# Optimization experiments

Measured on AMD Instinct MI355X. Metric: run time of the kernel, lower is better.

The kernel has to match this reference:

```python
import jax, jax.numpy as jnp
import numpy as np

K = 512       # embedding dim (also per-head dim in this quirky impl)
H = 8         # heads
NB = 4        # transformer blocks
VOCAB = 32000
BATCH = 4
T = 512
EPS = 1e-5


def setup_inputs() -> dict:
    key = jax.random.key(0)
    ks = jax.random.split(key, 16)
    s = 0.02
    f = jnp.float32
    return {
        "x": jax.random.randint(ks[0], (BATCH, T), 0, VOCAB, dtype=jnp.int64) if jax.config.jax_enable_x64 else jax.random.randint(ks[0], (BATCH, T), 0, VOCAB, dtype=jnp.int32),
        "embed_W": (jax.random.normal(ks[1], (VOCAB, K)) * s).astype(f),
        "Wq": (jax.random.normal(ks[2], (NB, K, K * H)) * s).astype(f),
        "Wk": (jax.random.normal(ks[3], (NB, K, K * H)) * s).astype(f),
        "Wv": (jax.random.normal(ks[4], (NB, K, K * H)) * s).astype(f),
        "Wu": (jax.random.normal(ks[5], (NB, K * H, K)) * s).astype(f),
        "bu": jnp.zeros((NB, K), f),
        "W1": (jax.random.normal(ks[6], (NB, K, 4 * K)) * s).astype(f),
        "b1": jnp.zeros((NB, 4 * K), f),
        "W2": (jax.random.normal(ks[7], (NB, 4 * K, K)) * s).astype(f),
        "b2": jnp.zeros((NB, K), f),
        "ln1_w": jnp.ones((NB, K), f), "ln1_b": jnp.zeros((NB, K), f),
        "ln2_w": jnp.ones((NB, K), f), "ln2_b": jnp.zeros((NB, K), f),
        "lnf_w": jnp.ones((K,), f),    "lnf_b": jnp.zeros((K,), f),
        "unembed_W": (jax.random.normal(ks[8], (K, VOCAB)) * s).astype(f),
        "unembed_b": jnp.zeros((VOCAB,), f),
    }


def _layernorm(x, w, b):
    m = jnp.mean(x, axis=-1, keepdims=True)
    v = jnp.mean((x - m) ** 2, axis=-1, keepdims=True)
    return (x - m) / jnp.sqrt(v + EPS) * w + b


def _pos_encoding(t, k):
    pos = jnp.arange(t, dtype=jnp.float32)[:, None]
    # faithful to source: div = 10000 ** (2 * arange(0,k,2) / k)
    div = 10000.0 ** (2.0 * jnp.arange(0, k, 2, dtype=jnp.float32) / k)
    ang = pos / div  # [t, k//2]
    y = jnp.zeros((t, k), jnp.float32)
    y = y.at[:, 0::2].set(jnp.sin(ang)).at[:, 1::2].set(jnp.cos(ang))
    return y


def _block(h, Wq, Wk, Wv, Wu, bu, W1, b1, W2, b2, ln1_w, ln1_b, ln2_w, ln2_b):
    b, t, k = h.shape
    q = (h @ Wq).reshape(b, t, H, k)
    kk = (h @ Wk).reshape(b, t, H, k)
    v = (h @ Wv).reshape(b, t, H, k)
    scores = jnp.einsum('bqhd,bshd->bhqs', q, kk) / (k ** 0.5)
    causal = jnp.tril(jnp.ones((t, t), bool))  # keep lower triangle
    scores = jnp.where(causal[None, None], scores, -jnp.inf)
    att = jax.nn.softmax(scores, axis=-1)
    y = jnp.einsum('bhqs,bshd->bqhd', att, v).reshape(b, t, H * k)
    y = y @ Wu + bu
    h = _layernorm(y + h, ln1_w, ln1_b)          # residual + norm1 (dropout off)
    ff = jax.nn.gelu(h @ W1 + b1, approximate=False) @ W2 + b2
    return _layernorm(ff + h, ln2_w, ln2_b)       # residual + norm2


def reference(x, embed_W, Wq, Wk, Wv, Wu, bu, W1, b1, W2, b2,
              ln1_w, ln1_b, ln2_w, ln2_b, lnf_w, lnf_b, unembed_W, unembed_b):
    b, t = x.shape
    h = embed_W[x] + _pos_encoding(t, K)
    for i in range(NB):
        h = _block(h, Wq[i], Wk[i], Wv[i], Wu[i], bu[i], W1[i], b1[i], W2[i], b2[i],
                   ln1_w[i], ln1_b[i], ln2_w[i], ln2_b[i])
    h = _layernorm(h, lnf_w, lnf_b)
    # torch does .squeeze(0): no-op for b>1, so output is [b, t, vocab]
    return h @ unembed_W + unembed_b
```

## Files before the change

kernel.cpp:

```cpp
#include <hip/hip_runtime.h>
#include <math.h>
#include <stdint.h>

#define KDIM 512
#define HEADS 8
#define NBLK 4
#define TSEQ 512
#define BATCH_ 4
#define ROWS 2048
#define DMODEL 4096
#define VOCAB_ 32000
#define FFDIM 2048

typedef __attribute__((ext_vector_type(4))) float f32x4;
typedef __attribute__((ext_vector_type(8))) short s16x8;
typedef unsigned short u16t;

__device__ __forceinline__ u16t f2bf(float f) {
    union { float f; unsigned u; } cv; cv.f = f;
    return (u16t)((cv.u + 0x7FFFu + ((cv.u >> 16) & 1u)) >> 16);
}

__device__ __forceinline__ void gload_lds16(const void* g, void* lds) {
    __builtin_amdgcn_global_load_lds(
        (const __attribute__((address_space(1))) unsigned int*)(uintptr_t)g,
        (__attribute__((address_space(3))) unsigned int*)(unsigned int)(uintptr_t)lds,
        16, 0, 0);
}

template<int BM, int BN, bool OUTBF, bool BIAS, bool GELU, bool MASK, bool KTRI>
__global__ __launch_bounds__(256, 2) void gemm_bf16(
    const u16t* __restrict__ A, const u16t* __restrict__ Bt,
    const float* __restrict__ bias, void* __restrict__ Cv,
    int Kd, int lda, int ldb, int ldc,
    long long aSB, long long aSH, long long bSB, long long bSH,
    long long cSB, long long cSH, int Hn, float scale)
{
    const int m0 = blockIdx.y * BM, n0 = blockIdx.x * BN;
    if (MASK && n0 > m0) return;

    const int zb = blockIdx.z / Hn, zh = blockIdx.z % Hn;
    A  += zb * aSB + zh * aSH;
    Bt += zb * bSB + zh * bSH;
    const int tid = threadIdx.x;
    const int wave = tid >> 6, lane = tid & 63;
    const int quad = lane >> 4, l15 = lane & 15;
    const int wm = (wave >> 1) * (BM / 2), wn = (wave & 1) * (BN / 2);
    constexpr int MT = BM / 32, NT = BN / 32;

    __shared__ __align__(16) u16t As[BM * 64];
    __shared__ __align__(16) u16t Bs[BN * 64];

    f32x4 acc[MT][NT];
    #pragma unroll
    for (int i = 0; i < MT; i++)
        #pragma unroll
        for (int j = 0; j < NT; j++)
            acc[i][j] = (f32x4){0.f, 0.f, 0.f, 0.f};

    const int kend = KTRI ? (Kd < m0 + BM ? Kd : m0 + BM) : Kd;

    for (int k0 = 0; k0 < kend; k0 += 64) {
        #pragma unroll
        for (int r = 0; r < BM / 32; ++r) {
            int cc = r * 256 + tid;
            int row = cc >> 3, pc = cc & 7;
            int kc = pc ^ (row & 7);
            gload_lds16(A + (long long)(m0 + row) * lda + k0 + kc * 8, &As[cc * 8]);
        }
        #pragma unroll
        for (int r = 0; r < BN / 32; ++r) {
            int cc = r * 256 + tid;
            int row = cc >> 3, pc = cc & 7;
            int kc = pc ^ (row & 7);
            gload_lds16(Bt + (long long)(n0 + row) * ldb + k0 + kc * 8, &Bs[cc * 8]);
        }
        __syncthreads();

        #pragma unroll
        for (int g = 0; g < 2; ++g) {
            s16x8 af[MT], bfr[NT];
            #pragma unroll
            for (int i = 0; i < MT; i++) {
                int row = wm + i * 16 + l15;
                int pc = (g * 4 + quad) ^ (row & 7);
                af[i] = *(const s16x8*)&As[row * 64 + pc * 8];
            }
            #pragma unroll
            for (int j = 0; j < NT; j++) {
                int row = wn + j * 16 + l15;
                int pc = (g * 4 + quad) ^ (row & 7);
                bfr[j] = *(const s16x8*)&Bs[row * 64 + pc * 8];
            }
            #pragma unroll
            for (int i = 0; i < MT; i++)
                #pragma unroll
                for (int j = 0; j < NT; j++)
                    acc[i][j] = __builtin_amdgcn_mfma_f32_16x16x32_bf16(
                        af[i], bfr[j], acc[i][j], 0, 0, 0);
        }
        __syncthreads();
    }

    const long long cb = zb * cSB + zh * cSH;
    #pragma unroll
    for (int i = 0; i < MT; i++) {
        #pragma unroll
        for (int j = 0; j < NT; j++) {
            const int col = n0 + wn + j * 16 + l15;
            #pragma unroll
            for (int r = 0; r < 4; r++) {
                const int row = m0 + wm + i * 16 + quad * 4 + r;
                float v = acc[i][j][r] * scale;
                if (BIAS) v += bias[col];
                if (GELU) v = 0.5f * v * (1.0f + erff(v * 0.70710678118654752f));
                if (OUTBF) ((u16t*)Cv)[cb + (long long)row * ldc + col] = f2bf(v);
                else       ((float*)Cv)[cb + (long long)row * ldc + col] = v;
            }
        }
    }
}

__global__ __launch_bounds__(256) void wconvT(
    const float* __restrict__ W, int ldw, int n_off, long long srcZ,
    u16t* __restrict__ WT, int ldt, long long dstZ)
{
    W  += (long long)blockIdx.z * srcZ;
    WT += (long long)blockIdx.z * dstZ;
    __shared__ float t[32][33];
    const int n0 = blockIdx.x * 32, k0 = blockIdx.y * 32;
    const int c = threadIdx.x & 31, r = threadIdx.x >> 5;
    #pragma unroll
    for (int i = 0; i < 4; i++)
        t[r + i * 8][c] = W[(long long)(k0 + r + i * 8) * ldw + n_off + n0 + c];
    __syncthreads();
    #pragma unroll
    for (int i = 0; i < 4; i++)
        WT[(long long)(n0 + r + i * 8) * ldt + k0 + c] = f2bf(t[c][r + i * 8]);
}

__global__ __launch_bounds__(256) void embed_pos(
    const int* __restrict__ x, const float* __restrict__ W,
    float* __restrict__ h, u16t* __restrict__ hb)
{
    int idx = blockIdx.x * 256 + threadIdx.x;
    int row = idx >> 9, c = idx & 511;
    int tpos = row & (TSEQ - 1);
    int tok = x[row];
    int i = c >> 1;
    float inv = expf(-9.210340371976184f * ((float)i * (1.0f / 128.0f)));
    float ang = (float)tpos * inv;
    float pe = (c & 1) ? cosf(ang) : sinf(ang);
    float v = W[(long long)tok * KDIM + c] + pe;
    h[idx] = v;
    hb[idx] = f2bf(v);
}

template<int NP, bool GB, bool RES>
__global__ __launch_bounds__(64) void ln512(
    const float* __restrict__ A, const float* __restrict__ R,
    const float* __restrict__ gb,
    const float* __restrict__ w, const float* __restrict__ bias,
    float* __restrict__ out, u16t* __restrict__ outb)
{
    long long row = blockIdx.x;
    int t = threadIdx.x;
    const float* a = A + row * KDIM;
    float4 u0 = *(const float4*)&a[t * 4];
    float4 u1 = *(const float4*)&a[256 + t * 4];
    if (NP == 2) {
        const float* a2 = A + (long long)ROWS * KDIM + row * KDIM;
        float4 p0 = *(const float4*)&a2[t * 4];
        float4 p1 = *(const float4*)&a2[256 + t * 4];
        u0.x += p0.x; u0.y += p0.y; u0.z += p0.z; u0.w += p0.w;
        u1.x += p1.x; u1.y += p1.y; u1.z += p1.z; u1.w += p1.w;
    }
    if (GB) {
        float4 g0 = *(const float4*)&gb[t * 4];
        float4 g1 = *(const float4*)&gb[256 + t * 4];
        u0.x += g0.x; u0.y += g0.y; u0.z += g0.z; u0.w += g0.w;
        u1.x += g1.x; u1.y += g1.y; u1.z += g1.z; u1.w += g1.w;
    }
    if (RES) {
        const float* rr = R + row * KDIM;
        float4 r0 = *(const float4*)&rr[t * 4];
        float4 r1 = *(const float4*)&rr[256 + t * 4];
        u0.x += r0.x; u0.y += r0.y; u0.z += r0.z; u0.w += r0.w;
        u1.x += r1.x; u1.y += r1.y; u1.z += r1.z; u1.w += r1.w;
    }
    float xv[8] = {u0.x, u0.y, u0.z, u0.w, u1.x, u1.y, u1.z, u1.w};
    float s = 0.f;
    #pragma unroll
    for (int e = 0; e < 8; e++) s += xv[e];
    #pragma unroll
    for (int off = 32; off; off >>= 1) s += __shfl_xor(s, off);
    float mean = s * (1.0f / 512.0f);
    float vs = 0.f;
    #pragma unroll
    for (int e = 0; e < 8; e++) { float d = xv[e] - mean; vs += d * d; }
    #pragma unroll
    for (int off = 32; off; off >>= 1) vs += __shfl_xor(vs, off);
    float rstd = rsqrtf(vs * (1.0f / 512.0f) + 1e-5f);

    int c0 = t * 4, c1 = 256 + t * 4;
    #pragma unroll
    for (int e = 0; e < 8; e++) {
        int c = (e < 4) ? (c0 + e) : (c1 + e - 4);
        float o = (xv[e] - mean) * rstd * w[c] + bias[c];
        out[row * KDIM + c] = o;
        outb[row * KDIM + c] = f2bf(o);
    }
}

__global__ __launch_bounds__(64) void softmax512b(
    const float* __restrict__ S, u16t* __restrict__ P)
{
    long long base = (long long)blockIdx.x * 512;
    const int r = blockIdx.x & (TSEQ - 1);
    int t = threadIdx.x;
    float4 u0 = *(const float4*)&S[base + t * 4];
    float4 u1 = *(const float4*)&S[base + 256 + t * 4];
    float xv[8] = {u0.x, u0.y, u0.z, u0.w, u1.x, u1.y, u1.z, u1.w};
    #pragma unroll
    for (int e = 0; e < 8; e++) {
        int c = (e < 4) ? (t * 4 + e) : (256 + t * 4 + e - 4);
        if (c > r) xv[e] = -1e30f;
    }
    float m = xv[0];
    #pragma unroll
    for (int e = 1; e < 8; e++) m = fmaxf(m, xv[e]);
    #pragma unroll
    for (int off = 32; off; off >>= 1) m = fmaxf(m, __shfl_xor(m, off));
    float s = 0.f;
    #pragma unroll
    for (int e = 0; e < 8; e++) { xv[e] = expf(xv[e] - m); s += xv[e]; }
    #pragma unroll
    for (int off = 32; off; off >>= 1) s += __shfl_xor(s, off);
    float inv = 1.0f / s;
    #pragma unroll
    for (int e = 0; e < 8; e++) {
        int c = (e < 4) ? (t * 4 + e) : (256 + t * 4 + e - 4);
        P[base + c] = f2bf(xv[e] * inv);
    }
}

extern "C" void kernel_launch(void* const* d_in, const int* in_sizes, int n_in,
                              void* d_out, int out_size, void* d_ws, size_t ws_size,
                              hipStream_t stream)
{
    const int*   x      = (const int*)  d_in[0];
    const float* embedW = (const float*)d_in[1];
    const float* Wq     = (const float*)d_in[2];
    const float* Wk     = (const float*)d_in[3];
    const float* Wv     = (const float*)d_in[4];
    const float* Wu     = (const float*)d_in[5];
    const float* bu     = (const float*)d_in[6];
    const float* W1     = (const float*)d_in[7];
    const float* b1     = (const float*)d_in[8];
    const float* W2     = (const float*)d_in[9];
    const float* b2     = (const float*)d_in[10];
    const float* ln1w   = (const float*)d_in[11];
    const float* ln1b   = (const float*)d_in[12];
    const float* ln2w   = (const float*)d_in[13];
    const float* ln2b   = (const float*)d_in[14];
    const float* lnfw   = (const float*)d_in[15];
    const float* lnfb   = (const float*)d_in[16];
    const float* unembW = (const float*)d_in[17];
    const float* unembB = (const float*)d_in[18];

    char* ob = (char*)d_out;
    float* outF = (float*)d_out;

    u16t*  wb  = (u16t*)(ob);
    u16t*  qk  = (u16t*)(ob + 83886080);
    u16t*  vt  = (u16t*)(ob + 117440512);
    float* sc  = (float*)(ob + 134217728);
    u16t*  Pb  = (u16t*) (ob + 167772160);
    u16t*  y   = (u16t*) (ob + 184549376);
    u16t*  f1  = (u16t*) (ob + 201326592);
    float* tmp = (float*)(ob + 209715200);
    float* ff2 = (float*)(ob + 218103808);
    float* h   = (float*)(ob + 226492416);
    float* h2  = (float*)(ob + 230686720);
    u16t*  hb  = (u16t*) (ob + 234881024);
    u16t*  h2b = (u16t*) (ob + 236978176);

    char* wsb = (char*)d_ws;
    u16t* hf  = (u16t*)(wsb);
    u16t* wun = (u16t*)(wsb + 2097152);

    const long long WBLK = 10485760;
    const long long OQ = 0, OK_ = 2097152, OV = 4194304, OU = 6291456,
                    O1 = 8388608, O2 = 9437184;

    const float inv_sqrt_k = 0.04419417382415922f;
    const long long z0 = 0;

    wconvT<<<dim3(DMODEL/32, KDIM/32, NBLK), 256, 0, stream>>>(
        Wq, DMODEL, 0, (long long)KDIM*DMODEL, wb + OQ, KDIM, WBLK);
    wconvT<<<dim3(DMODEL/32, KDIM/32, NBLK), 256, 0, stream>>>(
        Wk, DMODEL, 0, (long long)KDIM*DMODEL, wb + OK_, KDIM, WBLK);
    wconvT<<<dim3(DMODEL/32, KDIM/32, NBLK), 256, 0, stream>>>(
        Wv, DMODEL, 0, (long long)KDIM*DMODEL, wb + OV, KDIM, WBLK);
    wconvT<<<dim3(KDIM/32, DMODEL/32, NBLK), 256, 0, stream>>>(
        Wu, KDIM, 0, (long long)DMODEL*KDIM, wb + OU, DMODEL, WBLK);
    wconvT<<<dim3(FFDIM/32, KDIM/32, NBLK), 256, 0, stream>>>(
        W1, FFDIM, 0, (long long)KDIM*FFDIM, wb + O1, KDIM, WBLK);
    wconvT<<<dim3(KDIM/32, FFDIM/32, NBLK), 256, 0, stream>>>(
        W2, KDIM, 0, (long long)FFDIM*KDIM, wb + O2, FFDIM, WBLK);

    embed_pos<<<ROWS * KDIM / 256, 256, 0, stream>>>(x, embedW, h, hb);

    for (int i = 0; i < NBLK; i++) {
        u16t* wbi = wb + (long long)i * WBLK;

        gemm_bf16<128,128,true,false,false,false,false>
            <<<dim3(64, 16, 1), 256, 0, stream>>>(
            hb, wbi + OQ, nullptr, qk, KDIM, KDIM, KDIM, 2*DMODEL,
            z0,z0,z0,z0,z0,z0, 1, 1.0f);

        gemm_bf16<128,128,true,false,false,false,false>
            <<<dim3(16, 32, 1), 256, 0, stream>>>(
            wbi + OV, hb, nullptr, vt, KDIM, KDIM, KDIM, ROWS,
            z0,z0,z0,z0,z0,z0, 1, 1.0f);

        gemm_bf16<128,128,false,false,false,true,false>
            <<<dim3(4, 4, BATCH_*HEADS), 256, 0, stream>>>(
            qk, qk + DMODEL, nullptr, sc, KDIM, 2*DMODEL, 2*DMODEL, TSEQ,
            (long long)TSEQ*2*DMODEL, (long long)KDIM,
            (long long)TSEQ*2*DMODEL, (long long)KDIM,
            (long long)HEADS*TSEQ*TSEQ, (long long)TSEQ*TSEQ, HEADS, inv_sqrt_k);

        softmax512b<<<BATCH_*HEADS*TSEQ, 64, 0, stream>>>(sc, Pb);

        gemm_bf16<128,128,true,false,false,false,true>
            <<<dim3(4, 4, BATCH_*HEADS), 256, 0, stream>>>(
            Pb, vt, nullptr, y, TSEQ, TSEQ, ROWS, DMODEL,
            (long long)HEADS*TSEQ*TSEQ, (long long)TSEQ*TSEQ,
            (long long)TSEQ, (long long)TSEQ*ROWS,
            (long long)TSEQ*DMODEL, (long long)KDIM, HEADS, 1.0f);

        gemm_bf16<64,64,false,false,false,false,false>
            <<<dim3(8, 32, 2), 256, 0, stream>>>(
            y, wbi + OU, nullptr, tmp, DMODEL/2, DMODEL, DMODEL, KDIM,
            (long long)(DMODEL/2), z0, (long long)(DMODEL/2), z0,
            (long long)ROWS*KDIM, z0, 1, 1.0f);

        ln512<2,true,true><<<ROWS, 64, 0, stream>>>(
            tmp, h, bu + i*KDIM, ln1w + i*KDIM, ln1b + i*KDIM, h2, h2b);

        gemm_bf16<64,128,true,true,true,false,false>
            <<<dim3(16, 32, 1), 256, 0, stream>>>(
            h2b, wbi + O1, b1 + i*FFDIM, f1, KDIM, KDIM, KDIM, FFDIM,
            z0,z0,z0,z0,z0,z0, 1, 1.0f);

        gemm_bf16<64,64,false,false,false,false,false>
            <<<dim3(8, 32, 2), 256, 0, stream>>>(
            f1, wbi + O2, nullptr, ff2, FFDIM/2, FFDIM, FFDIM, KDIM,
            (long long)(FFDIM/2), z0, (long long)(FFDIM/2), z0,
            (long long)ROWS*KDIM, z0, 1, 1.0f);

        ln512<2,true,true><<<ROWS, 64, 0, stream>>>(
            ff2, h2, b2 + i*KDIM, ln2w + i*KDIM, ln2b + i*KDIM, h, hb);
    }

    ln512<1,false,false><<<ROWS, 64, 0, stream>>>(
        h, nullptr, nullptr, lnfw, lnfb, tmp, hf);

    const int CH = 6400;
    for (int c = 0; c < 5; c++) {
        wconvT<<<dim3(CH/32, KDIM/32, 1), 256, 0, stream>>>(
            unembW, VOCAB_, c*CH, z0, wun, KDIM, z0);
        gemm_bf16<128,128,false,true,false,false,false>
            <<<dim3(CH/128, 16, 1), 256, 0, stream>>>(
            hf, wun, unembB + c*CH, outF + c*CH, KDIM, KDIM, KDIM, VOCAB_,
            z0,z0,z0,z0,z0,z0, 1, 1.0f);
    }
}
```

Before: 1.182 ms.

## Fuse QKV projection and weight conversions, widen split-K, batch row kernels

Merges the Q/K and V-transpose projection GEMMs into one launch and the three Wq/Wk/Wv conversion kernels into one. The Wu projection moves to 128x128 tiles with split-K of 8 into the scores buffer, and LN1 sums the eight partials. LayerNorm and softmax now process four rows per 256-thread block. The diagonal-heavy P·V tiles are launched first (reversed row order). When workspace allows, unembedding runs as a single conversion and GEMM instead of five chunks. Together these cut launch count and tail effects, at the cost of more partial-sum traffic.

```diff
diff --git a/kernel.cpp b/kernel.cpp
--- a/kernel.cpp
+++ b/kernel.cpp
@@ -28,20 +28,13 @@
         16, 0, 0);
 }
 
-template<int BM, int BN, bool OUTBF, bool BIAS, bool GELU, bool MASK, bool KTRI>
-__global__ __launch_bounds__(256, 2) void gemm_bf16(
+template<int BM, int BN, bool OUTBF, bool BIAS, bool GELU, bool KTRI>
+__device__ __forceinline__ void gemm_body(
     const u16t* __restrict__ A, const u16t* __restrict__ Bt,
     const float* __restrict__ bias, void* __restrict__ Cv,
-    int Kd, int lda, int ldb, int ldc,
-    long long aSB, long long aSH, long long bSB, long long bSH,
-    long long cSB, long long cSH, int Hn, float scale)
-{
-    const int m0 = blockIdx.y * BM, n0 = blockIdx.x * BN;
-    if (MASK && n0 > m0) return;
-
-    const int zb = blockIdx.z / Hn, zh = blockIdx.z % Hn;
-    A  += zb * aSB + zh * aSH;
-    Bt += zb * bSB + zh * bSH;
+    int Kd, int lda, int ldb, int ldc, long long cb,
+    int m0, int n0, float scale)
+{
     const int tid = threadIdx.x;
     const int wave = tid >> 6, lane = tid & 63;
     const int quad = lane >> 4, l15 = lane & 15;
@@ -102,7 +95,6 @@
         __syncthreads();
     }
 
-    const long long cb = zb * cSB + zh * cSH;
     #pragma unroll
     for (int i = 0; i < MT; i++) {
         #pragma unroll
@@ -121,6 +113,42 @@
     }
 }
 
+template<int BM, int BN, bool OUTBF, bool BIAS, bool GELU, bool MASK, bool KTRI>
+__global__ __launch_bounds__(256, 2) void gemm_bf16(
+    const u16t* __restrict__ A, const u16t* __restrict__ Bt,
+    const float* __restrict__ bias, void* __restrict__ Cv,
+    int Kd, int lda, int ldb, int ldc,
+    long long aSB, long long aSH, long long bSB, long long bSH,
+    long long cSB, long long cSH, int Hn, float scale)
+{
+    const int by = KTRI ? (gridDim.y - 1 - blockIdx.y) : blockIdx.y;
+    const int m0 = by * BM, n0 = blockIdx.x * BN;
+    if (MASK && n0 > m0) return;
+    const int zb = blockIdx.z / Hn, zh = blockIdx.z % Hn;
+    gemm_body<BM, BN, OUTBF, BIAS, GELU, KTRI>(
+        A + zb * aSB + zh * aSH, Bt + zb * bSB + zh * bSH, bias, Cv,
+        Kd, lda, ldb, ldc, zb * cSB + zh * cSH, m0, n0, scale);
+}
+
+__global__ __launch_bounds__(256, 2) void gemm_qkvt(
+    const u16t* __restrict__ hb, const u16t* __restrict__ wq,
+    u16t* __restrict__ qk, const u16t* __restrict__ wv,
+    u16t* __restrict__ vt)
+{
+    const int bx = blockIdx.x;
+    const u16t* A; const u16t* Bt; u16t* C; int ldc, m0, n0;
+    if (bx < 1024) {
+        A = hb; Bt = wq; C = qk; ldc = 2 * DMODEL;
+        n0 = (bx & 63) * 128; m0 = (bx >> 6) * 128;
+    } else {
+        int i = bx - 1024;
+        A = wv; Bt = hb; C = vt; ldc = ROWS;
+        n0 = (i & 15) * 128; m0 = (i >> 4) * 128;
+    }
+    gemm_body<128, 128, true, false, false, false>(
+        A, Bt, nullptr, C, KDIM, KDIM, KDIM, ldc, 0, m0, n0, 1.0f);
+}
+
 __global__ __launch_bounds__(256) void wconvT(
     const float* __restrict__ W, int ldw, int n_off, long long srcZ,
     u16t* __restrict__ WT, int ldt, long long dstZ)
@@ -132,11 +160,31 @@
     const int c = threadIdx.x & 31, r = threadIdx.x >> 5;
     #pragma unroll
     for (int i = 0; i < 4; i++)
-        t[r + i * 8][c] = W[(long long)(k0 + r + i * 8) * ldw + n_off + n0 + c];
+        t[r + i * 8][c] = W[(long long)(k0 + r + i * 8) * ldw + n0 + c + n_off];
     __syncthreads();
     #pragma unroll
     for (int i = 0; i < 4; i++)
         WT[(long long)(n0 + r + i * 8) * ldt + k0 + c] = f2bf(t[c][r + i * 8]);
+}
+
+__global__ __launch_bounds__(256) void wconvT3(
+    const float* __restrict__ W0, const float* __restrict__ W1,
+    const float* __restrict__ W2, long long srcZ,
+    u16t* __restrict__ WT, long long dstZ, long long dstG)
+{
+    const int zi = blockIdx.z >> 2, zb = blockIdx.z & 3;
+    const float* W = (zi == 0 ? W0 : zi == 1 ? W1 : W2) + zb * srcZ;
+    u16t* D = WT + zi * dstG + zb * dstZ;
+    __shared__ float t[32][33];
+    const int n0 = blockIdx.x * 32, k0 = blockIdx.y * 32;
+    const int c = threadIdx.x & 31, r = threadIdx.x >> 5;
+    #pragma unroll
+    for (int i = 0; i < 4; i++)
+        t[r + i * 8][c] = W[(long long)(k0 + r + i * 8) * DMODEL + n0 + c];
+    __syncthreads();
+    #pragma unroll
+    for (int i = 0; i < 4; i++)
+        D[(long long)(n0 + r + i * 8) * KDIM + k0 + c] = f2bf(t[c][r + i * 8]);
 }
 
 __global__ __launch_bounds__(256) void embed_pos(
@@ -157,21 +205,22 @@
 }
 
 template<int NP, bool GB, bool RES>
-__global__ __launch_bounds__(64) void ln512(
+__global__ __launch_bounds__(256) void ln512(
     const float* __restrict__ A, const float* __restrict__ R,
     const float* __restrict__ gb,
     const float* __restrict__ w, const float* __restrict__ bias,
     float* __restrict__ out, u16t* __restrict__ outb)
 {
-    long long row = blockIdx.x;
-    int t = threadIdx.x;
+    const int wv = threadIdx.x >> 6, t = threadIdx.x & 63;
+    long long row = (long long)blockIdx.x * 4 + wv;
     const float* a = A + row * KDIM;
     float4 u0 = *(const float4*)&a[t * 4];
     float4 u1 = *(const float4*)&a[256 + t * 4];
-    if (NP == 2) {
-        const float* a2 = A + (long long)ROWS * KDIM + row * KDIM;
-        float4 p0 = *(const float4*)&a2[t * 4];
-        float4 p1 = *(const float4*)&a2[256 + t * 4];
+    #pragma unroll
+    for (int p = 1; p < NP; ++p) {
+        const float* ap = a + (long long)p * ROWS * KDIM;
+        float4 p0 = *(const float4*)&ap[t * 4];
+        float4 p1 = *(const float4*)&ap[256 + t * 4];
         u0.x += p0.x; u0.y += p0.y; u0.z += p0.z; u0.w += p0.w;
         u1.x += p1.x; u1.y += p1.y; u1.z += p1.z; u1.w += p1.w;
     }
@@ -212,12 +261,13 @@
     }
 }
 
-__global__ __launch_bounds__(64) void softmax512b(
+__global__ __launch_bounds__(256) void softmax512b(
     const float* __restrict__ S, u16t* __restrict__ P)
 {
-    long long base = (long long)blockIdx.x * 512;
-    const int r = blockIdx.x & (TSEQ - 1);
-    int t = threadIdx.x;
+    const int wv = threadIdx.x >> 6, t = threadIdx.x & 63;
+    long long row = (long long)blockIdx.x * 4 + wv;
+    long long base = row * 512;
+    const int r = (int)(row & (TSEQ - 1));
     float4 u0 = *(const float4*)&S[base + t * 4];
     float4 u1 = *(const float4*)&S[base + 256 + t * 4];
     float xv[8] = {u0.x, u0.y, u0.z, u0.w, u1.x, u1.y, u1.z, u1.w};
@@ -278,30 +328,26 @@
     u16t*  Pb  = (u16t*) (ob + 167772160);
     u16t*  y   = (u16t*) (ob + 184549376);
     u16t*  f1  = (u16t*) (ob + 201326592);
-    float* tmp = (float*)(ob + 209715200);
     float* ff2 = (float*)(ob + 218103808);
     float* h   = (float*)(ob + 226492416);
     float* h2  = (float*)(ob + 230686720);
     u16t*  hb  = (u16t*) (ob + 234881024);
     u16t*  h2b = (u16t*) (ob + 236978176);
+    float* tmp = sc;
 
     char* wsb = (char*)d_ws;
     u16t* hf  = (u16t*)(wsb);
     u16t* wun = (u16t*)(wsb + 2097152);
 
     const long long WBLK = 10485760;
-    const long long OQ = 0, OK_ = 2097152, OV = 4194304, OU = 6291456,
+    const long long OQ = 0, OV = 4194304, OU = 6291456,
                     O1 = 8388608, O2 = 9437184;
 
     const float inv_sqrt_k = 0.04419417382415922f;
     const long long z0 = 0;
 
-    wconvT<<<dim3(DMODEL/32, KDIM/32, NBLK), 256, 0, stream>>>(
-        Wq, DMODEL, 0, (long long)KDIM*DMODEL, wb + OQ, KDIM, WBLK);
-    wconvT<<<dim3(DMODEL/32, KDIM/32, NBLK), 256, 0, stream>>>(
-        Wk, DMODEL, 0, (long long)KDIM*DMODEL, wb + OK_, KDIM, WBLK);
-    wconvT<<<dim3(DMODEL/32, KDIM/32, NBLK), 256, 0, stream>>>(
-        Wv, DMODEL, 0, (long long)KDIM*DMODEL, wb + OV, KDIM, WBLK);
+    wconvT3<<<dim3(DMODEL/32, KDIM/32, 3*NBLK), 256, 0, stream>>>(
+        Wq, Wk, Wv, (long long)KDIM*DMODEL, wb, WBLK, 2097152);
     wconvT<<<dim3(KDIM/32, DMODEL/32, NBLK), 256, 0, stream>>>(
         Wu, KDIM, 0, (long long)DMODEL*KDIM, wb + OU, DMODEL, WBLK);
     wconvT<<<dim3(FFDIM/32, KDIM/32, NBLK), 256, 0, stream>>>(
@@ -314,15 +360,8 @@
     for (int i = 0; i < NBLK; i++) {
         u16t* wbi = wb + (long long)i * WBLK;
 
-        gemm_bf16<128,128,true,false,false,false,false>
-            <<<dim3(64, 16, 1), 256, 0, stream>>>(
-            hb, wbi + OQ, nullptr, qk, KDIM, KDIM, KDIM, 2*DMODEL,
-            z0,z0,z0,z0,z0,z0, 1, 1.0f);
-
-        gemm_bf16<128,128,true,false,false,false,false>
-            <<<dim3(16, 32, 1), 256, 0, stream>>>(
-            wbi + OV, hb, nullptr, vt, KDIM, KDIM, KDIM, ROWS,
-            z0,z0,z0,z0,z0,z0, 1, 1.0f);
+        gemm_qkvt<<<dim3(1536, 1, 1), 256, 0, stream>>>(
+            hb, wbi + OQ, qk, wbi + OV, vt);
 
         gemm_bf16<128,128,false,false,false,true,false>
             <<<dim3(4, 4, BATCH_*HEADS), 256, 0, stream>>>(
@@ -331,7 +370,7 @@
             (long long)TSEQ*2*DMODEL, (long long)KDIM,
             (long long)HEADS*TSEQ*TSEQ, (long long)TSEQ*TSEQ, HEADS, inv_sqrt_k);
 
-        softmax512b<<<BATCH_*HEADS*TSEQ, 64, 0, stream>>>(sc, Pb);
+        softmax512b<<<BATCH_*HEADS*TSEQ/4, 256, 0, stream>>>(sc, Pb);
 
         gemm_bf16<128,128,true,false,false,false,true>
             <<<dim3(4, 4, BATCH_*HEADS), 256, 0, stream>>>(
@@ -340,13 +379,13 @@
             (long long)TSEQ, (long long)TSEQ*ROWS,
             (long long)TSEQ*DMODEL, (long long)KDIM, HEADS, 1.0f);
 
-        gemm_bf16<64,64,false,false,false,false,false>
-            <<<dim3(8, 32, 2), 256, 0, stream>>>(
-            y, wbi + OU, nullptr, tmp, DMODEL/2, DMODEL, DMODEL, KDIM,
-            (long long)(DMODEL/2), z0, (long long)(DMODEL/2), z0,
+        gemm_bf16<128,128,false,false,false,false,false>
+            <<<dim3(4, 16, 8), 256, 0, stream>>>(
+            y, wbi + OU, nullptr, tmp, DMODEL/8, DMODEL, DMODEL, KDIM,
+            (long long)(DMODEL/8), z0, (long long)(DMODEL/8), z0,
             (long long)ROWS*KDIM, z0, 1, 1.0f);
 
-        ln512<2,true,true><<<ROWS, 64, 0, stream>>>(
+        ln512<8,true,true><<<ROWS/4, 256, 0, stream>>>(
             tmp, h, bu + i*KDIM, ln1w + i*KDIM, ln1b + i*KDIM, h2, h2b);
 
         gemm_bf16<64,128,true,true,true,false,false>
@@ -360,20 +399,29 @@
             (long long)(FFDIM/2), z0, (long long)(FFDIM/2), z0,
             (long long)ROWS*KDIM, z0, 1, 1.0f);
 
-        ln512<2,true,true><<<ROWS, 64, 0, stream>>>(
+        ln512<2,true,true><<<ROWS/4, 256, 0, stream>>>(
             ff2, h2, b2 + i*KDIM, ln2w + i*KDIM, ln2b + i*KDIM, h, hb);
     }
 
-    ln512<1,false,false><<<ROWS, 64, 0, stream>>>(
+    ln512<1,false,false><<<ROWS/4, 256, 0, stream>>>(
         h, nullptr, nullptr, lnfw, lnfb, tmp, hf);
 
-    const int CH = 6400;
-    for (int c = 0; c < 5; c++) {
-        wconvT<<<dim3(CH/32, KDIM/32, 1), 256, 0, stream>>>(
-            unembW, VOCAB_, c*CH, z0, wun, KDIM, z0);
+    if (ws_size >= (size_t)2097152 + (size_t)VOCAB_ * KDIM * 2) {
+        wconvT<<<dim3(VOCAB_/32, KDIM/32, 1), 256, 0, stream>>>(
+            unembW, VOCAB_, 0, z0, wun, KDIM, z0);
         gemm_bf16<128,128,false,true,false,false,false>
-            <<<dim3(CH/128, 16, 1), 256, 0, stream>>>(
-            hf, wun, unembB + c*CH, outF + c*CH, KDIM, KDIM, KDIM, VOCAB_,
+            <<<dim3(VOCAB_/128, 16, 1), 256, 0, stream>>>(
+            hf, wun, unembB, outF, KDIM, KDIM, KDIM, VOCAB_,
             z0,z0,z0,z0,z0,z0, 1, 1.0f);
-    }
-}
+    } else {
+        const int CH = 6400;
+        for (int c = 0; c < 5; c++) {
+            wconvT<<<dim3(CH/32, KDIM/32, 1), 256, 0, stream>>>(
+                unembW, VOCAB_, c*CH, z0, wun, KDIM, z0);
+            gemm_bf16<128,128,false,true,false,false,false>
+                <<<dim3(CH/128, 16, 1), 256, 0, stream>>>(
+                hf, wun, unembB + c*CH, outF + c*CH, KDIM, KDIM, KDIM, VOCAB_,
+                z0,z0,z0,z0,z0,z0, 1, 1.0f);
+        }
+    }
+}
```

New measurement: 1.119 ms. -5.4%, faster.
